# Optimization experiments

Measured on AMD Instinct MI355X. Metric: run time of the kernel, lower is better.

The kernel has to match this reference:

```python
import jax, jax.numpy as jnp
import numpy as np

LAMBDA_COORD = 5.0
LAMBDA_NOOBJ = 0.5
EPS = 1e-16


def setup_inputs() -> dict:
    key = jax.random.key(0)
    k1, k2, k3 = jax.random.split(key, 3)
    B, HW, C = 64, 6400, 85  # 80x80 grid, 5 + 80 classes
    T = 50                   # objects per image
    predictions = jax.random.normal(k1, (B, HW, C), dtype=jnp.float32)
    targets_box = jax.random.uniform(k2, (B, T, 4), dtype=jnp.float32)  # cx, cy, w, h in [0,1)
    targets_cls = jax.random.randint(k3, (B, T), 0, 80)
    return {
        "predictions": predictions,
        "targets_box": targets_box,
        "targets_cls": targets_cls,
        "grid_h": 80,
        "grid_w": 80,
    }


def reference(predictions, targets_box, targets_cls, grid_h, grid_w):
    B, HW, C = predictions.shape
    T = targets_box.shape[1]
    H, W = grid_h, grid_w

    cx, cy, w, h = (targets_box[..., i] for i in range(4))  # each [B, T]
    gxf = jnp.floor(cx * W)
    gyf = jnp.floor(cy * H)
    gi = (gyf * W + gxf).astype(jnp.int32)  # [B, T] grid cell index

    # gather predictions at assigned cells -> [B, T, C]
    g = jnp.take_along_axis(predictions, gi[:, :, None], axis=1)

    # coordinate losses (per-object mean over the 2 components, as F.mse_loss does)
    txy = jnp.stack([cx * W - gxf, cy * H - gyf], axis=-1)           # [B, T, 2]
    xy_loss = jnp.mean((jax.nn.sigmoid(g[..., :2]) - txy) ** 2, -1)  # [B, T]
    twh = jnp.log(jnp.stack([w * W, h * H], axis=-1) + EPS)
    wh_loss = jnp.mean((g[..., 2:4] - twh) ** 2, -1)

    # objectness BCE with target 1: -log(sigmoid(p)) = softplus(-p)
    conf_loss = jax.nn.softplus(-g[..., 4])

    # class cross-entropy
    logp = jax.nn.log_softmax(g[..., 5:], axis=-1)
    cls_loss = -jnp.take_along_axis(logp, targets_cls[..., None], axis=-1)[..., 0]

    per_obj = LAMBDA_COORD * (xy_loss + wh_loss) + conf_loss + cls_loss
    obj_sum = jnp.sum(per_obj)

    # no-object loss: mean BCE(sigmoid(conf), 0) = softplus(p) over cells without objects
    obj_mask = jnp.zeros((B, HW), dtype=bool).at[jnp.arange(B)[:, None], gi].set(True)
    noobj = ~obj_mask
    sp = jax.nn.softplus(predictions[..., 4])  # [B, HW]
    noobj_per_img = jnp.sum(sp * noobj, -1) / jnp.maximum(jnp.sum(noobj, -1), 1)
    noobj_sum = LAMBDA_NOOBJ * jnp.sum(noobj_per_img)

    num_objects = B * T  # all targets are in-grid by construction
    return (obj_sum + noobj_sum) / num_objects
```

## Files before the change

kernel.cpp:

```cpp
#include <hip/hip_runtime.h>
#include <math.h>

constexpr int B_  = 64;
constexpr int HW_ = 6400;
constexpr int C_  = 85;
constexpr int T_  = 50;
constexpr int H_  = 80;
constexpr int W_  = 80;
constexpr float LC    = 5.0f;
constexpr float LN    = 0.5f;
constexpr float INV_N = 1.0f / (B_ * T_);
constexpr int SUBN  = 4;
constexpr int CHUNK = HW_ / SUBN;

constexpr int OFF_PEROBJ = 0;
constexpr int OFF_MSP    = OFF_PEROBJ + B_ * T_;
constexpr int OFF_CANON  = OFF_MSP + B_ * T_;
constexpr int OFF_PART   = OFF_CANON + B_ * T_;
constexpr int OFF_IMG    = OFF_PART + B_ * SUBN;

__device__ __forceinline__ float softplus_f(float x) {
    return fmaxf(x, 0.0f) + log1pf(expf(-fabsf(x)));
}

__global__ __launch_bounds__(256) void obj_kernel(
    const float* __restrict__ pred, const float* __restrict__ tbox,
    const int* __restrict__ tcls,
    float* __restrict__ per_obj, float* __restrict__ masked_sp,
    float* __restrict__ canon)
{
    int gid  = blockIdx.x * blockDim.x + threadIdx.x;
    int obj  = gid >> 6;
    int lane = threadIdx.x & 63;
    if (obj >= B_ * T_) return;
    int b   = obj / T_;
    int myt = obj % T_;

    const float4 tb = ((const float4*)tbox)[obj];
    float gxf = floorf(tb.x * (float)W_);
    float gyf = floorf(tb.y * (float)H_);
    int gi = (int)(gyf * (float)W_ + gxf);

    bool dup = false;
    if (lane < T_) {
        const float4 to = ((const float4*)tbox)[b * T_ + lane];
        int gio = (int)(floorf(to.y * (float)H_) * (float)W_ +
                        floorf(to.x * (float)W_));
        dup = (lane < myt) && (gio == gi);
    }
    bool canonical = (__ballot(dup) == 0ULL);

    const float* g = pred + ((size_t)b * HW_ + gi) * C_;
    int cls = tcls[obj];

    int   c2 = lane + 64;
    float v1 = g[lane];
    float v2 = (c2 < C_) ? g[c2] : 0.0f;

    float m = -1e30f;
    if (lane >= 5) m = v1;
    if (c2 < C_)   m = fmaxf(m, v2);
    #pragma unroll
    for (int off = 32; off; off >>= 1) m = fmaxf(m, __shfl_xor(m, off, 64));
    float s = 0.0f;
    if (lane >= 5) s += expf(v1 - m);
    if (c2 < C_)   s += expf(v2 - m);
    #pragma unroll
    for (int off = 32; off; off >>= 1) s += __shfl_xor(s, off, 64);
    float lse = m + logf(s);

    float contrib = 0.0f;
    if (lane == 0) {
        float d = 1.0f / (1.0f + expf(-v1)) - (tb.x * (float)W_ - gxf);
        contrib = LC * 0.5f * d * d;
    } else if (lane == 1) {
        float d = 1.0f / (1.0f + expf(-v1)) - (tb.y * (float)H_ - gyf);
        contrib = LC * 0.5f * d * d;
    } else if (lane == 2) {
        float d = v1 - logf(tb.z * (float)W_ + 1e-16f);
        contrib = LC * 0.5f * d * d;
    } else if (lane == 3) {
        float d = v1 - logf(tb.w * (float)H_ + 1e-16f);
        contrib = LC * 0.5f * d * d;
    } else if (lane == 4) {
        contrib = softplus_f(-v1);
        masked_sp[obj] = canonical ? softplus_f(v1) : 0.0f;
    }
    if (lane == 5 + cls) contrib += lse - v1;
    if (c2   == 5 + cls) contrib += lse - v2;

    #pragma unroll
    for (int off = 32; off; off >>= 1) contrib += __shfl_xor(contrib, off, 64);
    if (lane == 0) {
        per_obj[obj] = contrib;
        canon[obj]   = canonical ? 1.0f : 0.0f;
    }
}

__global__ __launch_bounds__(256) void conf_partial(
    const float* __restrict__ pred, float* __restrict__ img_part)
{
    int b    = blockIdx.x / SUBN;
    int sub  = blockIdx.x % SUBN;
    int base = sub * CHUNK;
    const float* p = pred + (size_t)b * HW_ * C_;

    float sum = 0.0f;
    for (int i = base + (int)threadIdx.x; i < base + CHUNK; i += 256)
        sum += softplus_f(p[(size_t)i * C_ + 4]);
    #pragma unroll
    for (int off = 32; off; off >>= 1) sum += __shfl_xor(sum, off, 64);

    __shared__ float ss[4];
    int wid = threadIdx.x >> 6;
    if ((threadIdx.x & 63) == 0) ss[wid] = sum;
    __syncthreads();
    if (threadIdx.x == 0)
        img_part[blockIdx.x] = ss[0] + ss[1] + ss[2] + ss[3];
}

__global__ __launch_bounds__(64) void per_image(
    const float* __restrict__ per_obj, const float* __restrict__ masked_sp,
    const float* __restrict__ canon, const float* __restrict__ img_part,
    float* __restrict__ img_result)
{
    int b = blockIdx.x;
    int t = threadIdx.x;

    float po  = (t < T_)   ? per_obj[b * T_ + t]    : 0.0f;
    float msp = (t < T_)   ? masked_sp[b * T_ + t]  : 0.0f;
    float cn  = (t < T_)   ? canon[b * T_ + t]      : 0.0f;
    float tp  = (t < SUBN) ? img_part[b * SUBN + t] : 0.0f;
    #pragma unroll
    for (int off = 32; off; off >>= 1) {
        po  += __shfl_xor(po,  off, 64);
        msp += __shfl_xor(msp, off, 64);
        cn  += __shfl_xor(cn,  off, 64);
        tp  += __shfl_xor(tp,  off, 64);
    }
    if (t == 0) {
        float n_noobj = fmaxf((float)HW_ - cn, 1.0f);
        float noobj   = LN * (tp - msp) / n_noobj;
        img_result[b] = po + noobj;
    }
}

__global__ __launch_bounds__(64) void final_k(
    const float* __restrict__ img_result, float* __restrict__ out)
{
    float v = img_result[threadIdx.x];
    #pragma unroll
    for (int off = 32; off; off >>= 1) v += __shfl_xor(v, off, 64);
    if (threadIdx.x == 0) out[0] = v * INV_N;
}

extern "C" void kernel_launch(void* const* d_in, const int* in_sizes, int n_in,
                              void* d_out, int out_size, void* d_ws, size_t ws_size,
                              hipStream_t stream) {
    const float* pred = (const float*)d_in[0];
    const float* tbox = (const float*)d_in[1];
    const int*   tcls = (const int*)d_in[2];
    float* out = (float*)d_out;

    float* ws        = (float*)d_ws;
    float* per_obj   = ws + OFF_PEROBJ;
    float* masked_sp = ws + OFF_MSP;
    float* canon     = ws + OFF_CANON;
    float* img_part  = ws + OFF_PART;
    float* img_res   = ws + OFF_IMG;

    obj_kernel  <<<(B_ * T_ * 64 + 255) / 256, 256, 0, stream>>>(
        pred, tbox, tcls, per_obj, masked_sp, canon);
    conf_partial<<<B_ * SUBN, 256, 0, stream>>>(pred, img_part);
    per_image   <<<B_, 64, 0, stream>>>(per_obj, masked_sp, canon, img_part, img_res);
    final_k     <<<1, 64, 0, stream>>>(img_res, out);
}
```

Measured before the change: 23.09 us.

## Merge object and confidence kernels into one launch and fuse final reductions

The per-object loss kernel and the confidence softplus partial-sum kernel now run as one launch, with block index choosing the role, so the two independent workloads overlap on the GPU. The confidence reduction is split into 16 chunks per image instead of 4, giving more blocks to hide strided-load latency. The per-image and final reductions are merged into a single 256-thread block. This cuts the launch count from four to two, at the cost of a few more partial sums to combine.

```diff
diff --git a/kernel.cpp b/kernel.cpp
--- a/kernel.cpp
+++ b/kernel.cpp
@@ -10,148 +10,154 @@
 constexpr float LC    = 5.0f;
 constexpr float LN    = 0.5f;
 constexpr float INV_N = 1.0f / (B_ * T_);
-constexpr int SUBN  = 4;
-constexpr int CHUNK = HW_ / SUBN;
+
+constexpr int OBJ_BLOCKS  = (B_ * T_) / 4;
+constexpr int SUBN        = 16;
+constexpr int CONF_BLOCKS = B_ * SUBN;
+constexpr int CHUNK       = HW_ / SUBN;
 
 constexpr int OFF_PEROBJ = 0;
 constexpr int OFF_MSP    = OFF_PEROBJ + B_ * T_;
 constexpr int OFF_CANON  = OFF_MSP + B_ * T_;
 constexpr int OFF_PART   = OFF_CANON + B_ * T_;
-constexpr int OFF_IMG    = OFF_PART + B_ * SUBN;
 
 __device__ __forceinline__ float softplus_f(float x) {
     return fmaxf(x, 0.0f) + log1pf(expf(-fabsf(x)));
 }
 
-__global__ __launch_bounds__(256) void obj_kernel(
+__global__ __launch_bounds__(256) void main_kernel(
     const float* __restrict__ pred, const float* __restrict__ tbox,
     const int* __restrict__ tcls,
     float* __restrict__ per_obj, float* __restrict__ masked_sp,
-    float* __restrict__ canon)
+    float* __restrict__ canon, float* __restrict__ img_part)
 {
-    int gid  = blockIdx.x * blockDim.x + threadIdx.x;
-    int obj  = gid >> 6;
-    int lane = threadIdx.x & 63;
-    if (obj >= B_ * T_) return;
-    int b   = obj / T_;
-    int myt = obj % T_;
+    if (blockIdx.x < OBJ_BLOCKS) {
+        int gid  = blockIdx.x * 256 + threadIdx.x;
+        int obj  = gid >> 6;
+        int lane = threadIdx.x & 63;
+        int b   = obj / T_;
+        int myt = obj % T_;
 
-    const float4 tb = ((const float4*)tbox)[obj];
-    float gxf = floorf(tb.x * (float)W_);
-    float gyf = floorf(tb.y * (float)H_);
-    int gi = (int)(gyf * (float)W_ + gxf);
+        const float4 tb = ((const float4*)tbox)[obj];
+        float gxf = floorf(tb.x * (float)W_);
+        float gyf = floorf(tb.y * (float)H_);
+        int gi = (int)(gyf * (float)W_ + gxf);
 
-    bool dup = false;
-    if (lane < T_) {
-        const float4 to = ((const float4*)tbox)[b * T_ + lane];
-        int gio = (int)(floorf(to.y * (float)H_) * (float)W_ +
-                        floorf(to.x * (float)W_));
-        dup = (lane < myt) && (gio == gi);
-    }
-    bool canonical = (__ballot(dup) == 0ULL);
+        bool dup = false;
+        if (lane < T_) {
+            const float4 to = ((const float4*)tbox)[b * T_ + lane];
+            int gio = (int)(floorf(to.y * (float)H_) * (float)W_ +
+                            floorf(to.x * (float)W_));
+            dup = (lane < myt) && (gio == gi);
+        }
+        bool canonical = (__ballot(dup) == 0ULL);
 
-    const float* g = pred + ((size_t)b * HW_ + gi) * C_;
-    int cls = tcls[obj];
+        const float* g = pred + ((size_t)b * HW_ + gi) * C_;
+        int cls = tcls[obj];
 
-    int   c2 = lane + 64;
-    float v1 = g[lane];
-    float v2 = (c2 < C_) ? g[c2] : 0.0f;
+        int   c2 = lane + 64;
+        float v1 = g[lane];
+        float v2 = (c2 < C_) ? g[c2] : 0.0f;
 
-    float m = -1e30f;
-    if (lane >= 5) m = v1;
-    if (c2 < C_)   m = fmaxf(m, v2);
-    #pragma unroll
-    for (int off = 32; off; off >>= 1) m = fmaxf(m, __shfl_xor(m, off, 64));
-    float s = 0.0f;
-    if (lane >= 5) s += expf(v1 - m);
-    if (c2 < C_)   s += expf(v2 - m);
-    #pragma unroll
-    for (int off = 32; off; off >>= 1) s += __shfl_xor(s, off, 64);
-    float lse = m + logf(s);
+        float m = -1e30f;
+        if (lane >= 5) m = v1;
+        if (c2 < C_)   m = fmaxf(m, v2);
+        #pragma unroll
+        for (int off = 32; off; off >>= 1) m = fmaxf(m, __shfl_xor(m, off, 64));
+        float s = 0.0f;
+        if (lane >= 5) s += expf(v1 - m);
+        if (c2 < C_)   s += expf(v2 - m);
+        #pragma unroll
+        for (int off = 32; off; off >>= 1) s += __shfl_xor(s, off, 64);
+        float lse = m + logf(s);
 
-    float contrib = 0.0f;
-    if (lane == 0) {
-        float d = 1.0f / (1.0f + expf(-v1)) - (tb.x * (float)W_ - gxf);
-        contrib = LC * 0.5f * d * d;
-    } else if (lane == 1) {
-        float d = 1.0f / (1.0f + expf(-v1)) - (tb.y * (float)H_ - gyf);
-        contrib = LC * 0.5f * d * d;
-    } else if (lane == 2) {
-        float d = v1 - logf(tb.z * (float)W_ + 1e-16f);
-        contrib = LC * 0.5f * d * d;
-    } else if (lane == 3) {
-        float d = v1 - logf(tb.w * (float)H_ + 1e-16f);
-        contrib = LC * 0.5f * d * d;
-    } else if (lane == 4) {
-        contrib = softplus_f(-v1);
-        masked_sp[obj] = canonical ? softplus_f(v1) : 0.0f;
-    }
-    if (lane == 5 + cls) contrib += lse - v1;
-    if (c2   == 5 + cls) contrib += lse - v2;
+        float contrib = 0.0f;
+        if (lane == 0) {
+            float d = 1.0f / (1.0f + expf(-v1)) - (tb.x * (float)W_ - gxf);
+            contrib = LC * 0.5f * d * d;
+        } else if (lane == 1) {
+            float d = 1.0f / (1.0f + expf(-v1)) - (tb.y * (float)H_ - gyf);
+            contrib = LC * 0.5f * d * d;
+        } else if (lane == 2) {
+            float d = v1 - logf(tb.z * (float)W_ + 1e-16f);
+            contrib = LC * 0.5f * d * d;
+        } else if (lane == 3) {
+            float d = v1 - logf(tb.w * (float)H_ + 1e-16f);
+            contrib = LC * 0.5f * d * d;
+        } else if (lane == 4) {
+            contrib = softplus_f(-v1);
+            masked_sp[obj] = canonical ? softplus_f(v1) : 0.0f;
+        }
+        if (lane == 5 + cls) contrib += lse - v1;
+        if (c2   == 5 + cls) contrib += lse - v2;
 
-    #pragma unroll
-    for (int off = 32; off; off >>= 1) contrib += __shfl_xor(contrib, off, 64);
-    if (lane == 0) {
-        per_obj[obj] = contrib;
-        canon[obj]   = canonical ? 1.0f : 0.0f;
+        #pragma unroll
+        for (int off = 32; off; off >>= 1) contrib += __shfl_xor(contrib, off, 64);
+        if (lane == 0) {
+            per_obj[obj] = contrib;
+            canon[obj]   = canonical ? 1.0f : 0.0f;
+        }
+    } else {
+        int c    = blockIdx.x - OBJ_BLOCKS;
+        int b    = c >> 4;
+        int sub  = c & 15;
+        int base = sub * CHUNK;
+        const float* p = pred + (size_t)b * HW_ * C_;
+
+        float sum = 0.0f;
+        for (int i = base + (int)threadIdx.x; i < base + CHUNK; i += 256)
+            sum += softplus_f(p[(size_t)i * C_ + 4]);
+        #pragma unroll
+        for (int off = 32; off; off >>= 1) sum += __shfl_xor(sum, off, 64);
+
+        __shared__ float ss[4];
+        int wid = threadIdx.x >> 6;
+        if ((threadIdx.x & 63) == 0) ss[wid] = sum;
+        __syncthreads();
+        if (threadIdx.x == 0)
+            img_part[c] = ss[0] + ss[1] + ss[2] + ss[3];
     }
 }
 
-__global__ __launch_bounds__(256) void conf_partial(
-    const float* __restrict__ pred, float* __restrict__ img_part)
-{
-    int b    = blockIdx.x / SUBN;
-    int sub  = blockIdx.x % SUBN;
-    int base = sub * CHUNK;
-    const float* p = pred + (size_t)b * HW_ * C_;
-
-    float sum = 0.0f;
-    for (int i = base + (int)threadIdx.x; i < base + CHUNK; i += 256)
-        sum += softplus_f(p[(size_t)i * C_ + 4]);
-    #pragma unroll
-    for (int off = 32; off; off >>= 1) sum += __shfl_xor(sum, off, 64);
-
-    __shared__ float ss[4];
-    int wid = threadIdx.x >> 6;
-    if ((threadIdx.x & 63) == 0) ss[wid] = sum;
-    __syncthreads();
-    if (threadIdx.x == 0)
-        img_part[blockIdx.x] = ss[0] + ss[1] + ss[2] + ss[3];
-}
-
-__global__ __launch_bounds__(64) void per_image(
+__global__ __launch_bounds__(256) void combine_kernel(
     const float* __restrict__ per_obj, const float* __restrict__ masked_sp,
     const float* __restrict__ canon, const float* __restrict__ img_part,
-    float* __restrict__ img_result)
+    float* __restrict__ out)
 {
-    int b = blockIdx.x;
     int t = threadIdx.x;
+    int b = t >> 2;
+    int q = t & 3;
 
-    float po  = (t < T_)   ? per_obj[b * T_ + t]    : 0.0f;
-    float msp = (t < T_)   ? masked_sp[b * T_ + t]  : 0.0f;
-    float cn  = (t < T_)   ? canon[b * T_ + t]      : 0.0f;
-    float tp  = (t < SUBN) ? img_part[b * SUBN + t] : 0.0f;
+    float po = 0.0f, msp = 0.0f, cn = 0.0f, tp = 0.0f;
+    for (int i = q; i < T_; i += 4) {
+        po  += per_obj[b * T_ + i];
+        msp += masked_sp[b * T_ + i];
+        cn  += canon[b * T_ + i];
+    }
+    for (int j = q; j < SUBN; j += 4)
+        tp += img_part[b * SUBN + j];
+
     #pragma unroll
-    for (int off = 32; off; off >>= 1) {
+    for (int off = 1; off <= 2; off <<= 1) {
         po  += __shfl_xor(po,  off, 64);
         msp += __shfl_xor(msp, off, 64);
         cn  += __shfl_xor(cn,  off, 64);
         tp  += __shfl_xor(tp,  off, 64);
     }
-    if (t == 0) {
+
+    __shared__ float simg[B_];
+    if (q == 0) {
         float n_noobj = fmaxf((float)HW_ - cn, 1.0f);
-        float noobj   = LN * (tp - msp) / n_noobj;
-        img_result[b] = po + noobj;
+        simg[b] = po + LN * (tp - msp) / n_noobj;
     }
-}
+    __syncthreads();
 
-__global__ __launch_bounds__(64) void final_k(
-    const float* __restrict__ img_result, float* __restrict__ out)
-{
-    float v = img_result[threadIdx.x];
-    #pragma unroll
-    for (int off = 32; off; off >>= 1) v += __shfl_xor(v, off, 64);
-    if (threadIdx.x == 0) out[0] = v * INV_N;
+    if (t < 64) {
+        float v = simg[t];
+        #pragma unroll
+        for (int off = 32; off; off >>= 1) v += __shfl_xor(v, off, 64);
+        if (t == 0) out[0] = v * INV_N;
+    }
 }
 
 extern "C" void kernel_launch(void* const* d_in, const int* in_sizes, int n_in,
@@ -167,11 +173,8 @@
     float* masked_sp = ws + OFF_MSP;
     float* canon     = ws + OFF_CANON;
     float* img_part  = ws + OFF_PART;
-    float* img_res   = ws + OFF_IMG;
 
-    obj_kernel  <<<(B_ * T_ * 64 + 255) / 256, 256, 0, stream>>>(
-        pred, tbox, tcls, per_obj, masked_sp, canon);
-    conf_partial<<<B_ * SUBN, 256, 0, stream>>>(pred, img_part);
-    per_image   <<<B_, 64, 0, stream>>>(per_obj, masked_sp, canon, img_part, img_res);
-    final_k     <<<1, 64, 0, stream>>>(img_res, out);
+    main_kernel<<<OBJ_BLOCKS + CONF_BLOCKS, 256, 0, stream>>>(
+        pred, tbox, tcls, per_obj, masked_sp, canon, img_part);
+    combine_kernel<<<1, 256, 0, stream>>>(per_obj, masked_sp, canon, img_part, out);
 }
```

Result: faster. 19.96 us (-13.6%).
